# Kernel tuning notes

Hardware: AMD Instinct MI355X
Metric: run time of the kernel (lower is better)

Reference implementation:

```python
import jax, jax.numpy as jnp
import numpy as np

NEG_SLOPE = 0.2  # PyG GATConv default negative_slope


def gat_conv(x, src, dst, W, a_src, a_dst, b, N):
    """Single PyG-style GATConv (add_self_loops already applied via src/dst).
    x: [N, F_in], W: [F_in, H*C], a_src/a_dst: [H, C], b: [H*C].
    Returns [N, H*C] (concat=True)."""
    H, C = a_src.shape
    h = (x @ W).reshape(N, H, C)                      # [N,H,C]
    alpha_src = jnp.sum(h * a_src[None], axis=-1)      # [N,H]
    alpha_dst = jnp.sum(h * a_dst[None], axis=-1)      # [N,H]
    e = jax.nn.leaky_relu(alpha_src[src] + alpha_dst[dst], NEG_SLOPE)  # [E,H]
    # numerically stable segment softmax over incoming edges of each dst node
    m = jax.ops.segment_max(e, dst, num_segments=N)    # [N,H]
    m = jnp.where(jnp.isfinite(m), m, 0.0)
    ex = jnp.exp(e - m[dst])                           # [E,H]
    den = jax.ops.segment_sum(ex, dst, num_segments=N) # [N,H]
    alpha = ex / (den[dst] + 1e-16)                    # [E,H]
    out = jax.ops.segment_sum(h[src] * alpha[..., None], dst, num_segments=N)  # [N,H,C]
    return out.reshape(N, H * C) + b


def setup_inputs() -> dict:
    key = jax.random.key(0)
    ks = jax.random.split(key, 9)
    B, N, E = 2, 50000, 800000
    d_model, n_hidden, en_dim, H = 128, 128, 64, 1
    fea_mats = jax.random.normal(ks[0], (B, N, d_model), dtype=jnp.float32)
    edge_index = jax.random.randint(ks[1], (B, 2, E), 0, N, dtype=jnp.int32)
    s1 = 1.0 / np.sqrt(d_model)
    s2 = 1.0 / np.sqrt(n_hidden)
    return {
        "fea_mats": fea_mats,
        "edge_index": edge_index,
        "W1": jax.random.normal(ks[2], (d_model, H * n_hidden), dtype=jnp.float32) * s1,
        "att_src1": jax.random.normal(ks[3], (H, n_hidden), dtype=jnp.float32) * s2,
        "att_dst1": jax.random.normal(ks[4], (H, n_hidden), dtype=jnp.float32) * s2,
        "b1": jnp.zeros((H * n_hidden,), dtype=jnp.float32),
        "W2": jax.random.normal(ks[5], (H * n_hidden, H * en_dim), dtype=jnp.float32) * s2,
        "att_src2": jax.random.normal(ks[6], (H, en_dim), dtype=jnp.float32) / np.sqrt(en_dim),
        "att_dst2": jax.random.normal(ks[7], (H, en_dim), dtype=jnp.float32) / np.sqrt(en_dim),
        "b2": jnp.zeros((H * en_dim,), dtype=jnp.float32),
    }


def reference(fea_mats, edge_index, W1, att_src1, att_dst1, b1, W2, att_src2, att_dst2, b2):
    B, N, _ = fea_mats.shape
    loops = jnp.arange(N, dtype=edge_index.dtype)

    def per_graph(x, ei):
        # PyG GATConv adds self-loops by default
        src = jnp.concatenate([ei[0], loops])
        dst = jnp.concatenate([ei[1], loops])
        h = gat_conv(x, src, dst, W1, att_src1, att_dst1, b1, N)
        h = jax.nn.relu(h)
        h = gat_conv(h, src, dst, W2, att_src2, att_dst2, b2, N)
        return h  # [N, en_dim]

    return jax.vmap(per_graph)(fea_mats, edge_index)  # [B, N, en_dim]
```

## Files before the change

kernel.cpp:

```cpp
#include <hip/hip_runtime.h>

#define NEG_SLOPE 0.2f
static constexpr int BLK = 256;
static constexpr int EPB = 4096;
static constexpr int CAP = 6144;

typedef short bf16x8 __attribute__((ext_vector_type(8)));
typedef float f32x4  __attribute__((ext_vector_type(4)));
typedef unsigned short u16x8 __attribute__((ext_vector_type(8)));
typedef unsigned short u16x4 __attribute__((ext_vector_type(4)));

static inline int cdiv(long a, long b){ return (int)((a + b - 1) / b); }

__device__ __forceinline__ unsigned short f2bf(float f){
    unsigned u = __float_as_uint(f);
    u += 0x7fff + ((u >> 16) & 1);
    return (unsigned short)(u >> 16);
}
__device__ __forceinline__ float bf2f(unsigned short h){
    return __uint_as_float(((unsigned)h) << 16);
}
__device__ __forceinline__ float lrelu(float v){
    return v > 0.f ? v : NEG_SLOPE * v;
}

struct GP {
    const int* src; const int* dst; const float* X;
    int* gcnt; int* gbase; int* ebuf; int* rowptr; int* csrsrc;
    unsigned short* h1b; float* agg1; unsigned short* h2b;
    float *as1, *ad1, *as2, *ad2; float* outp;
};

template<int CO, int CT, bool RELU_IN, bool BF16OUT>
__device__ __forceinline__ void gemm_dev(
    int bid, const float* __restrict__ X,
    const unsigned short* __restrict__ Wt_hi, const unsigned short* __restrict__ Wt_lo,
    const float* __restrict__ avs, const float* __restrict__ avd,
    void* __restrict__ Hout, float* __restrict__ as_out, float* __restrict__ ad_out,
    int N, unsigned short* smem)
{
    constexpr int CHUNKS = CO / (CT * 16);
    constexpr int HWB = CT * 4096;
    int ch, rtb;
    if (CHUNKS == 1){ ch = 0; rtb = bid; } else { ch = bid & 1; rtb = bid >> 1; }
    int c0 = ch * (CT * 16);

    {
        const char* srch = (const char*)(Wt_hi + (size_t)c0 * 128);
        const char* srcl = (const char*)(Wt_lo + (size_t)c0 * 128);
        #pragma unroll
        for (int it = 0; it < CT * 2; ++it){
            int o = (it * 256 + (int)threadIdx.x) * 16;
            const char* sp = (o < HWB) ? (srch + o) : (srcl + (o - HWB));
            u16x8 v = *(const u16x8*)sp;
            int so = o ^ (((o >> 8) & 7) << 4);
            *(u16x8*)((char*)smem + so) = v;
        }
    }
    __syncthreads();

    int wave = threadIdx.x >> 6;
    int lane = threadIdx.x & 63;
    int rt = rtb * 4 + wave;
    if (rt >= (N >> 4)) return;
    int r0 = rt << 4;
    int rl = lane & 15, g = lane >> 4;
    const float* xrow = X + (long)(r0 + rl) * 128 + g * 8;

    f32x4 acc[CT];
    #pragma unroll
    for (int t = 0; t < CT; t++) acc[t] = (f32x4)(0.f);

    int sw = (rl & 7) << 4;
    #pragma unroll
    for (int ks = 0; ks < 4; ks++){
        float4 xa = *(const float4*)(xrow + ks * 32);
        float4 xb = *(const float4*)(xrow + ks * 32 + 4);
        float xv[8] = {xa.x, xa.y, xa.z, xa.w, xb.x, xb.y, xb.z, xb.w};
        bf16x8 xbf;
        #pragma unroll
        for (int j = 0; j < 8; j++){
            float x = xv[j];
            if (RELU_IN) x = fmaxf(x, 0.f);
            xbf[j] = (short)f2bf(x);
        }
        int rbase = rl * 256 + ks * 64 + g * 16;
        #pragma unroll
        for (int t = 0; t < CT; t++){
            bf16x8 wh = *(const bf16x8*)((char*)smem + ((t * 4096 + rbase) ^ sw));
            bf16x8 wl = *(const bf16x8*)((char*)smem + ((HWB + t * 4096 + rbase) ^ sw));
            acc[t] = __builtin_amdgcn_mfma_f32_16x16x32_bf16(wh, xbf, acc[t], 0, 0, 0);
            acc[t] = __builtin_amdgcn_mfma_f32_16x16x32_bf16(wl, xbf, acc[t], 0, 0, 0);
        }
    }

    float ps = 0.f, pd = 0.f;
    #pragma unroll
    for (int t = 0; t < CT; t++){
        int c = c0 + t * 16 + 4 * g;
        float4 vs4 = *(const float4*)(avs + c);
        float4 vd4 = *(const float4*)(avd + c);
        ps += acc[t][0]*vs4.x + acc[t][1]*vs4.y + acc[t][2]*vs4.z + acc[t][3]*vs4.w;
        pd += acc[t][0]*vd4.x + acc[t][1]*vd4.y + acc[t][2]*vd4.z + acc[t][3]*vd4.w;
        long base = (long)(r0 + rl) * CO + c;
        if (BF16OUT){
            u16x4 pk;
            #pragma unroll
            for (int r = 0; r < 4; r++) pk[r] = f2bf(acc[t][r]);
            *(u16x4*)((unsigned short*)Hout + base) = pk;
        } else {
            float4 pv;
            pv.x = acc[t][0]; pv.y = acc[t][1]; pv.z = acc[t][2]; pv.w = acc[t][3];
            *(float4*)((float*)Hout + base) = pv;
        }
    }
    ps += __shfl_xor(ps, 16, 64); ps += __shfl_xor(ps, 32, 64);
    pd += __shfl_xor(pd, 16, 64); pd += __shfl_xor(pd, 32, 64);
    if (g == 0){
        unsafeAtomicAdd(as_out + r0 + rl, ps);
        unsafeAtomicAdd(ad_out + r0 + rl, pd);
    }
}

__device__ __forceinline__ void bucket_dev(
    int bid, const GP* __restrict__ g, int E, int Etot, int nbk, unsigned short* smem)
{
    int* spk   = (int*)smem;
    int* shist = spk + 4096;
    int* sbase = shist + 256;
    int tid = (int)threadIdx.x;
    for (int i = tid; i < nbk; i += 256) shist[i] = 0;
    __syncthreads();
    int e0 = bid * EPB;
    #pragma unroll
    for (int i = 0; i < EPB / 256; i++){
        int idx = i * 256 + tid; int e = e0 + idx;
        unsigned p = 0xFFFFFFFFu;
        if (e < Etot){
            int s, d;
            if (e < E){ s = g->src[e]; d = g->dst[e]; } else { s = e - E; d = s; }
            p = ((unsigned)s << 16) | (unsigned)d;
            atomicAdd(&shist[d >> 8], 1);
        }
        spk[idx] = (int)p;
    }
    __syncthreads();
    for (int i = tid; i < nbk; i += 256){
        sbase[i] = atomicAdd(&g->gcnt[i], shist[i]);
        shist[i] = 0;
    }
    __syncthreads();
    #pragma unroll
    for (int i = 0; i < EPB / 256; i++){
        int idx = i * 256 + tid;
        unsigned p = (unsigned)spk[idx];
        if (p != 0xFFFFFFFFu){
            int d = (int)(p & 0xFFFFu); int b = d >> 8;
            int r = sbase[b] + atomicAdd(&shist[b], 1);
            if (r < CAP) g->ebuf[(size_t)b * CAP + r] = (int)p;
        }
    }
}

__device__ __forceinline__ void fine_dev(int k, const GP* __restrict__ g, int N, int Etot)
{
    __shared__ int pk2[CAP];
    __shared__ int fs[256];
    __shared__ int fill[256];
    __shared__ int fh[256];
    int tid = (int)threadIdx.x;
    int cnt = min(g->gcnt[k], CAP);
    int bb  = g->gbase[k];
    for (int i = tid; i < cnt; i += 256) pk2[i] = g->ebuf[(size_t)k * CAP + i];
    fh[tid] = 0; fill[tid] = 0;
    __syncthreads();
    for (int i = tid; i < cnt; i += 256) atomicAdd(&fh[pk2[i] & 255], 1);
    __syncthreads();
    int v = fh[tid];
    fs[tid] = v;
    __syncthreads();
    #pragma unroll
    for (int off = 1; off < 256; off <<= 1){
        int t = (tid >= off) ? fs[tid - off] : 0;
        __syncthreads();
        fs[tid] += t;
        __syncthreads();
    }
    int excl = fs[tid] - v;
    __syncthreads();
    fs[tid] = excl;
    __syncthreads();
    int node = k * 256 + tid;
    if (node < N) g->rowptr[node] = bb + excl;
    if (k == 0 && tid == 0) g->rowptr[N] = Etot;
    for (int i = tid; i < cnt; i += 256){
        unsigned p = (unsigned)pk2[i];
        int f = (int)(p & 255u);
        int r = atomicAdd(&fill[f], 1);
        g->csrsrc[bb + fs[f] + r] = (int)(p >> 16);
    }
}

template<int CO>
__device__ __forceinline__ void agg_dev(
    int bid, const int* __restrict__ rowptr, const int* __restrict__ csr_src,
    const float* __restrict__ as, const float* __restrict__ ad,
    const unsigned short* __restrict__ hb, const float* __restrict__ bias,
    float* __restrict__ out, int N)
{
    constexpr int GRP = (CO == 128) ? 16 : 8;
    constexpr int ELEMS = 8;
    constexpr int NPB = 256 / GRP;
    using uvec = u16x8;
    int tid = (int)threadIdx.x;
    int grp = tid / GRP;
    int ql  = tid % GRP;
    int node = bid * NPB + grp;
    if (node >= N) return;
    int start = rowptr[node];
    int deg   = rowptr[node + 1] - start;
    float adv = ad[node];

    int sv[4]; float ev[4];
    #pragma unroll
    for (int q = 0; q < 4; q++){
        int idx = q * GRP + ql;
        sv[q] = 0; ev[q] = -1e30f;
        if (idx < deg){ sv[q] = csr_src[start + idx]; ev[q] = lrelu(as[sv[q]] + adv); }
    }
    float m = fmaxf(fmaxf(ev[0], ev[1]), fmaxf(ev[2], ev[3]));
    if (deg > 4 * GRP){
        for (int j = 4 * GRP + ql; j < deg; j += GRP)
            m = fmaxf(m, lrelu(as[csr_src[start + j]] + adv));
    }
    #pragma unroll
    for (int off = GRP >> 1; off; off >>= 1) m = fmaxf(m, __shfl_xor(m, off, GRP));

    float xq[4]; float sum = 0.f;
    #pragma unroll
    for (int q = 0; q < 4; q++){
        xq[q] = (q * GRP + ql < deg) ? __expf(ev[q] - m) : 0.f;
        sum += xq[q];
    }
    if (deg > 4 * GRP){
        for (int j = 4 * GRP + ql; j < deg; j += GRP)
            sum += __expf(lrelu(as[csr_src[start + j]] + adv) - m);
    }
    #pragma unroll
    for (int off = GRP >> 1; off; off >>= 1) sum += __shfl_xor(sum, off, GRP);
    float inv = 1.f / (sum + 1e-16f);
    float av[4];
    #pragma unroll
    for (int q = 0; q < 4; q++) av[q] = xq[q] * inv;

    float acc[ELEMS];
    #pragma unroll
    for (int i = 0; i < ELEMS; i++) acc[i] = 0.f;

    #pragma unroll
    for (int q = 0; q < 4; q++){
        int rem = deg - q * GRP;
        if (rem <= 0) break;
        int lim = rem < GRP ? rem : GRP;
        float aq = av[q]; int sq = sv[q];
        int t = 0;
        for (; t + 7 < lim; t += 8){
            int   s0 = __shfl(sq, t+0, GRP), s1 = __shfl(sq, t+1, GRP);
            int   s2 = __shfl(sq, t+2, GRP), s3 = __shfl(sq, t+3, GRP);
            int   s4 = __shfl(sq, t+4, GRP), s5 = __shfl(sq, t+5, GRP);
            int   s6 = __shfl(sq, t+6, GRP), s7 = __shfl(sq, t+7, GRP);
            float a0 = __shfl(aq, t+0, GRP), a1 = __shfl(aq, t+1, GRP);
            float a2 = __shfl(aq, t+2, GRP), a3 = __shfl(aq, t+3, GRP);
            float a4 = __shfl(aq, t+4, GRP), a5 = __shfl(aq, t+5, GRP);
            float a6 = __shfl(aq, t+6, GRP), a7 = __shfl(aq, t+7, GRP);
            uvec r0 = *(const uvec*)(hb + (long)s0 * CO + ql * ELEMS);
            uvec r1 = *(const uvec*)(hb + (long)s1 * CO + ql * ELEMS);
            uvec r2 = *(const uvec*)(hb + (long)s2 * CO + ql * ELEMS);
            uvec r3 = *(const uvec*)(hb + (long)s3 * CO + ql * ELEMS);
            uvec r4 = *(const uvec*)(hb + (long)s4 * CO + ql * ELEMS);
            uvec r5 = *(const uvec*)(hb + (long)s5 * CO + ql * ELEMS);
            uvec r6 = *(const uvec*)(hb + (long)s6 * CO + ql * ELEMS);
            uvec r7 = *(const uvec*)(hb + (long)s7 * CO + ql * ELEMS);
            #pragma unroll
            for (int i = 0; i < ELEMS; i++)
                acc[i] += a0 * bf2f(r0[i]) + a1 * bf2f(r1[i])
                        + a2 * bf2f(r2[i]) + a3 * bf2f(r3[i])
                        + a4 * bf2f(r4[i]) + a5 * bf2f(r5[i])
                        + a6 * bf2f(r6[i]) + a7 * bf2f(r7[i]);
        }
        for (; t + 3 < lim; t += 4){
            int   s0 = __shfl(sq, t+0, GRP), s1 = __shfl(sq, t+1, GRP);
            int   s2 = __shfl(sq, t+2, GRP), s3 = __shfl(sq, t+3, GRP);
            float a0 = __shfl(aq, t+0, GRP), a1 = __shfl(aq, t+1, GRP);
            float a2 = __shfl(aq, t+2, GRP), a3 = __shfl(aq, t+3, GRP);
            uvec r0 = *(const uvec*)(hb + (long)s0 * CO + ql * ELEMS);
            uvec r1 = *(const uvec*)(hb + (long)s1 * CO + ql * ELEMS);
            uvec r2 = *(const uvec*)(hb + (long)s2 * CO + ql * ELEMS);
            uvec r3 = *(const uvec*)(hb + (long)s3 * CO + ql * ELEMS);
            #pragma unroll
            for (int i = 0; i < ELEMS; i++)
                acc[i] += a0 * bf2f(r0[i]) + a1 * bf2f(r1[i])
                        + a2 * bf2f(r2[i]) + a3 * bf2f(r3[i]);
        }
        for (; t < lim; t++){
            int   s0 = __shfl(sq, t, GRP);
            float a0 = __shfl(aq, t, GRP);
            uvec r0 = *(const uvec*)(hb + (long)s0 * CO + ql * ELEMS);
            #pragma unroll
            for (int i = 0; i < ELEMS; i++) acc[i] += a0 * bf2f(r0[i]);
        }
        if (lim < GRP) break;
    }
    if (deg > 4 * GRP){
        for (int j = 4 * GRP; j < deg; j++){
            int sj = csr_src[start + j];
            float aj = __expf(lrelu(as[sj] + adv) - m) * inv;
            uvec r0 = *(const uvec*)(hb + (long)sj * CO + ql * ELEMS);
            #pragma unroll
            for (int i = 0; i < ELEMS; i++) acc[i] += aj * bf2f(r0[i]);
        }
    }

    float* o = out + (long)node * CO + ql * ELEMS;
    #pragma unroll
    for (int i = 0; i < ELEMS; i += 4){
        float4 ov;
        ov.x = acc[i+0] + bias[ql * ELEMS + i + 0];
        ov.y = acc[i+1] + bias[ql * ELEMS + i + 1];
        ov.z = acc[i+2] + bias[ql * ELEMS + i + 2];
        ov.w = acc[i+3] + bias[ql * ELEMS + i + 3];
        *(float4*)(o + i) = ov;
    }
}

__global__ __launch_bounds__(BLK) void prep_k(
    const float* __restrict__ W1, const float* __restrict__ W2,
    unsigned short* __restrict__ w1h, unsigned short* __restrict__ w1l,
    unsigned short* __restrict__ w2h, unsigned short* __restrict__ w2l)
{
    int i = blockIdx.x * BLK + threadIdx.x;
    if (i < 128 * 128){
        int c = i >> 7, k = i & 127;
        float w = W1[k * 128 + c];
        unsigned short hi = f2bf(w);
        w1h[i] = hi; w1l[i] = f2bf(w - bf2f(hi));
        if (i < 64 * 128){
            float w2 = W2[k * 64 + c];
            unsigned short hi2 = f2bf(w2);
            w2h[i] = hi2; w2l[i] = f2bf(w2 - bf2f(hi2));
        }
    }
}

__global__ __launch_bounds__(256, 4) void kA(
    GP a, GP b, const unsigned short* __restrict__ w1h, const unsigned short* __restrict__ w1l,
    const float* __restrict__ avs1, const float* __restrict__ avd1,
    int EB_a, int EB_b, int GB_a, int GB_b, int E, int Etot, int N, int nbk)
{
    __shared__ unsigned short smem[16384];
    int bid = blockIdx.x;
    if (bid < EB_a){ bucket_dev(bid, &a, E, Etot, nbk, smem); return; }
    bid -= EB_a;
    if (bid < EB_b){ bucket_dev(bid, &b, E, Etot, nbk, smem); return; }
    bid -= EB_b;
    if (bid < GB_a){ gemm_dev<128,4,false,true>(bid, a.X, w1h, w1l, avs1, avd1, a.h1b, a.as1, a.ad1, N, smem); return; }
    bid -= GB_a;
    if (bid < GB_b) gemm_dev<128,4,false,true>(bid, b.X, w1h, w1l, avs1, avd1, b.h1b, b.as1, b.ad1, N, smem);
}

__global__ __launch_bounds__(256) void kscan(GP a, GP b, int nbk){
    const GP* g = (blockIdx.x == 0) ? &a : &b;
    __shared__ int sh[256];
    int tid = (int)threadIdx.x;
    int v = (tid < nbk) ? g->gcnt[tid] : 0;
    sh[tid] = v;
    __syncthreads();
    #pragma unroll
    for (int off = 1; off < 256; off <<= 1){
        int t = (tid >= off) ? sh[tid - off] : 0;
        __syncthreads();
        sh[tid] += t;
        __syncthreads();
    }
    if (tid < nbk) g->gbase[tid] = sh[tid] - v;
}

__global__ __launch_bounds__(256) void kB(GP a, GP b, int nb_a, int nb_b, int N, int Etot){
    int bid = blockIdx.x; const GP* g; int k;
    if (bid < nb_a){ g = &a; k = bid; }
    else { k = bid - nb_a; if (k >= nb_b) return; g = &b; }
    fine_dev(k, g, N, Etot);
}

__global__ __launch_bounds__(256, 4) void gemm2_k(
    GP a, GP b, const unsigned short* __restrict__ w2h, const unsigned short* __restrict__ w2l,
    const float* __restrict__ avs2, const float* __restrict__ avd2, int GB_a, int GB_b, int N)
{
    __shared__ unsigned short smem[8192];
    int bid = blockIdx.x;
    if (bid < GB_a) gemm_dev<64,2,true,true>(bid, a.agg1, w2h, w2l, avs2, avd2, a.h2b, a.as2, a.ad2, N, smem);
    else { bid -= GB_a; if (bid < GB_b) gemm_dev<64,2,true,true>(bid, b.agg1, w2h, w2l, avs2, avd2, b.h2b, b.as2, b.ad2, N, smem); }
}

template<int CO>
__global__ __launch_bounds__(BLK) void agg2_k(GP a, GP b, const float* bias, int AB_a, int AB_b, int N){
    int bid = blockIdx.x; const GP* g; int lb;
    if (bid < AB_a){ g = &a; lb = bid; }
    else { lb = bid - AB_a; if (lb >= AB_b) return; g = &b; }
    const float* as; const float* ad; const unsigned short* h; float* outp;
    if constexpr (CO == 128){ as = g->as1; ad = g->ad1; h = g->h1b; outp = g->agg1; }
    else                    { as = g->as2; ad = g->ad2; h = g->h2b; outp = g->outp; }
    agg_dev<CO>(lb, g->rowptr, g->csrsrc, as, ad, h, bias, outp, N);
}

extern "C" void kernel_launch(void* const* d_in, const int* in_sizes, int n_in,
                              void* d_out, int out_size, void* d_ws, size_t ws_size,
                              hipStream_t stream)
{
    const float* fea  = (const float*)d_in[0];
    const int*   ei   = (const int*)  d_in[1];
    const float* W1   = (const float*)d_in[2];
    const float* av_s1= (const float*)d_in[3];
    const float* av_d1= (const float*)d_in[4];
    const float* b1   = (const float*)d_in[5];
    const float* W2   = (const float*)d_in[6];
    const float* av_s2= (const float*)d_in[7];
    const float* av_d2= (const float*)d_in[8];
    const float* b2   = (const float*)d_in[9];
    float* out = (float*)d_out;

    const int B = 2;
    const int N = out_size / (B * 64);
    const int E = in_sizes[1] / (2 * B);
    const int Etot = E + N;
    const int nbk = (N + 255) >> 8;

    size_t pg = 256 + (size_t)nbk * CAP + (size_t)(N + 2) + (size_t)Etot
              + (size_t)N * (64 + 128 + 32);
    size_t wtf = 8192 + 8192 + 4096 + 4096;
    auto total_f = [&](int ng){ return wtf + (size_t)ng * (4 * (size_t)N + 256) + (size_t)ng * pg + 64; };
    bool fused = (ws_size >= total_f(2) * sizeof(float));
    int NG = fused ? 2 : 1;

    float* ws = (float*)d_ws;
    size_t off = 0;
    unsigned short* w1h = (unsigned short*)(ws + off); off += 8192;
    unsigned short* w1l = (unsigned short*)(ws + off); off += 8192;
    unsigned short* w2h = (unsigned short*)(ws + off); off += 4096;
    unsigned short* w2l = (unsigned short*)(ws + off); off += 4096;

    float* zbase = ws + off;
    size_t znum = (size_t)NG * (4 * (size_t)N + 256);
    off += znum;

    GP g[2];
    for (int gi = 0; gi < NG; gi++){
        GP p;
        p.as1  = zbase + (size_t)gi * (4 * (size_t)N + 256);
        p.ad1  = p.as1 + N;
        p.as2  = p.ad1 + N;
        p.ad2  = p.as2 + N;
        p.gcnt = (int*)(p.ad2 + N);
        p.gbase  = (int*)(ws + off); off += 256;
        p.ebuf   = (int*)(ws + off); off += (size_t)nbk * CAP;
        p.rowptr = (int*)(ws + off); off += (size_t)(N + 2);
        p.csrsrc = (int*)(ws + off); off += Etot;
        p.h1b  = (unsigned short*)(ws + off); off += (size_t)N * 64;
        p.agg1 = ws + off; off += (size_t)N * 128;
        p.h2b  = (unsigned short*)(ws + off); off += (size_t)N * 32;
        g[gi] = p;
    }

    const int RT  = N >> 4;
    const int GB1 = cdiv(RT, 4) * 2;
    const int GB2 = cdiv(RT, 4) * 2;
    const int EBk = cdiv(Etot, EPB);
    const int AB1 = cdiv(N, 16);
    const int AB2 = cdiv(N, 32);

    if (fused){
        for (int bi = 0; bi < 2; bi++){
            g[bi].src = ei + (size_t)bi * 2 * E;
            g[bi].dst = g[bi].src + E;
            g[bi].X   = fea + (size_t)bi * N * 128;
            g[bi].outp= out + (size_t)bi * N * 64;
        }
        hipMemsetAsync(zbase, 0, znum * sizeof(float), stream);
        prep_k<<<cdiv(128*128, BLK), BLK, 0, stream>>>(W1, W2, w1h, w1l, w2h, w2l);
        kA<<<2*EBk + 2*GB1, 256, 0, stream>>>(g[0], g[1], w1h, w1l, av_s1, av_d1,
                                              EBk, EBk, GB1, GB1, E, Etot, N, nbk);
        kscan<<<2, 256, 0, stream>>>(g[0], g[1], nbk);
        kB<<<2*nbk, 256, 0, stream>>>(g[0], g[1], nbk, nbk, N, Etot);
        agg2_k<128><<<2*AB1, BLK, 0, stream>>>(g[0], g[1], b1, AB1, AB1, N);
        gemm2_k <<<2*GB2, 256, 0, stream>>>(g[0], g[1], w2h, w2l, av_s2, av_d2, GB2, GB2, N);
        agg2_k<64> <<<2*AB2, BLK, 0, stream>>>(g[0], g[1], b2, AB2, AB2, N);
    } else {
        prep_k<<<cdiv(128*128, BLK), BLK, 0, stream>>>(W1, W2, w1h, w1l, w2h, w2l);
        for (int bi = 0; bi < B; bi++){
            GP p = g[0];
            p.src = ei + (size_t)bi * 2 * E;
            p.dst = p.src + E;
            p.X   = fea + (size_t)bi * N * 128;
            p.outp= out + (size_t)bi * N * 64;
            hipMemsetAsync(zbase, 0, znum * sizeof(float), stream);
            kA<<<EBk + GB1, 256, 0, stream>>>(p, p, w1h, w1l, av_s1, av_d1,
                                              EBk, 0, GB1, 0, E, Etot, N, nbk);
            kscan<<<1, 256, 0, stream>>>(p, p, nbk);
            kB<<<nbk, 256, 0, stream>>>(p, p, nbk, 0, N, Etot);
            agg2_k<128><<<AB1, BLK, 0, stream>>>(p, p, b1, AB1, 0, N);
            gemm2_k <<<GB2, 256, 0, stream>>>(p, p, w2h, w2l, av_s2, av_d2, GB2, 0, N);
            agg2_k<64> <<<AB2, BLK, 0, stream>>>(p, p, b2, AB2, 0, N);
        }
    }
}
```

Measured before the change: 223.6 us.

## Fuse layer-1 aggregation with layer-2 GEMM via LDS MFMA tile

The layer-1 aggregation kernel now applies bias and ReLU, stores the 16-node result tile in LDS as bf16, and multiplies it directly by W2 using MFMA. It writes h2 in bf16 and accumulates the layer-2 attention logits with atomics. This removes the fp32 agg1 intermediate buffer, its global write and read, and one kernel launch. The 8-wide unrolled gather loop is also dropped in favour of the 4-wide path. The trade-offs are extra MFMA work and W2 loads in every aggregation block, atomic contention on as2/ad2, and possibly less memory-level parallelism in the gather.

After: 204.2 us. 8.7% less time.

```diff
diff --git a/kernel.cpp b/kernel.cpp
--- a/kernel.cpp
+++ b/kernel.cpp
@@ -27,7 +27,7 @@
 struct GP {
     const int* src; const int* dst; const float* X;
     int* gcnt; int* gbase; int* ebuf; int* rowptr; int* csrsrc;
-    unsigned short* h1b; float* agg1; unsigned short* h2b;
+    unsigned short* h1b; unsigned short* h2b;
     float *as1, *ad1, *as2, *ad2; float* outp;
 };
 
@@ -201,22 +201,12 @@
     }
 }
 
-template<int CO>
-__device__ __forceinline__ void agg_dev(
-    int bid, const int* __restrict__ rowptr, const int* __restrict__ csr_src,
+template<int CO, int GRP>
+__device__ __forceinline__ void agg_core(
+    const int* __restrict__ rowptr, const int* __restrict__ csr_src,
     const float* __restrict__ as, const float* __restrict__ ad,
-    const unsigned short* __restrict__ hb, const float* __restrict__ bias,
-    float* __restrict__ out, int N)
-{
-    constexpr int GRP = (CO == 128) ? 16 : 8;
-    constexpr int ELEMS = 8;
-    constexpr int NPB = 256 / GRP;
-    using uvec = u16x8;
-    int tid = (int)threadIdx.x;
-    int grp = tid / GRP;
-    int ql  = tid % GRP;
-    int node = bid * NPB + grp;
-    if (node >= N) return;
+    const unsigned short* __restrict__ hb, int node, int ql, float* acc)
+{
     int start = rowptr[node];
     int deg   = rowptr[node + 1] - start;
     float adv = ad[node];
@@ -249,65 +239,37 @@
     #pragma unroll
     for (int off = GRP >> 1; off; off >>= 1) sum += __shfl_xor(sum, off, GRP);
     float inv = 1.f / (sum + 1e-16f);
-    float av[4];
-    #pragma unroll
-    for (int q = 0; q < 4; q++) av[q] = xq[q] * inv;
-
-    float acc[ELEMS];
-    #pragma unroll
-    for (int i = 0; i < ELEMS; i++) acc[i] = 0.f;
+
+    #pragma unroll
+    for (int i = 0; i < 8; i++) acc[i] = 0.f;
 
     #pragma unroll
     for (int q = 0; q < 4; q++){
         int rem = deg - q * GRP;
         if (rem <= 0) break;
         int lim = rem < GRP ? rem : GRP;
-        float aq = av[q]; int sq = sv[q];
+        float aq = xq[q] * inv; int sq = sv[q];
         int t = 0;
-        for (; t + 7 < lim; t += 8){
-            int   s0 = __shfl(sq, t+0, GRP), s1 = __shfl(sq, t+1, GRP);
-            int   s2 = __shfl(sq, t+2, GRP), s3 = __shfl(sq, t+3, GRP);
-            int   s4 = __shfl(sq, t+4, GRP), s5 = __shfl(sq, t+5, GRP);
-            int   s6 = __shfl(sq, t+6, GRP), s7 = __shfl(sq, t+7, GRP);
-            float a0 = __shfl(aq, t+0, GRP), a1 = __shfl(aq, t+1, GRP);
-            float a2 = __shfl(aq, t+2, GRP), a3 = __shfl(aq, t+3, GRP);
-            float a4 = __shfl(aq, t+4, GRP), a5 = __shfl(aq, t+5, GRP);
-            float a6 = __shfl(aq, t+6, GRP), a7 = __shfl(aq, t+7, GRP);
-            uvec r0 = *(const uvec*)(hb + (long)s0 * CO + ql * ELEMS);
-            uvec r1 = *(const uvec*)(hb + (long)s1 * CO + ql * ELEMS);
-            uvec r2 = *(const uvec*)(hb + (long)s2 * CO + ql * ELEMS);
-            uvec r3 = *(const uvec*)(hb + (long)s3 * CO + ql * ELEMS);
-            uvec r4 = *(const uvec*)(hb + (long)s4 * CO + ql * ELEMS);
-            uvec r5 = *(const uvec*)(hb + (long)s5 * CO + ql * ELEMS);
-            uvec r6 = *(const uvec*)(hb + (long)s6 * CO + ql * ELEMS);
-            uvec r7 = *(const uvec*)(hb + (long)s7 * CO + ql * ELEMS);
-            #pragma unroll
-            for (int i = 0; i < ELEMS; i++)
-                acc[i] += a0 * bf2f(r0[i]) + a1 * bf2f(r1[i])
-                        + a2 * bf2f(r2[i]) + a3 * bf2f(r3[i])
-                        + a4 * bf2f(r4[i]) + a5 * bf2f(r5[i])
-                        + a6 * bf2f(r6[i]) + a7 * bf2f(r7[i]);
-        }
         for (; t + 3 < lim; t += 4){
             int   s0 = __shfl(sq, t+0, GRP), s1 = __shfl(sq, t+1, GRP);
             int   s2 = __shfl(sq, t+2, GRP), s3 = __shfl(sq, t+3, GRP);
             float a0 = __shfl(aq, t+0, GRP), a1 = __shfl(aq, t+1, GRP);
             float a2 = __shfl(aq, t+2, GRP), a3 = __shfl(aq, t+3, GRP);
-            uvec r0 = *(const uvec*)(hb + (long)s0 * CO + ql * ELEMS);
-            uvec r1 = *(const uvec*)(hb + (long)s1 * CO + ql * ELEMS);
-            uvec r2 = *(const uvec*)(hb + (long)s2 * CO + ql * ELEMS);
-            uvec r3 = *(const uvec*)(hb + (long)s3 * CO + ql * ELEMS);
+            u16x8 r0 = *(const u16x8*)(hb + (long)s0 * CO + ql * 8);
+            u16x8 r1 = *(const u16x8*)(hb + (long)s1 * CO + ql * 8);
+            u16x8 r2 = *(const u16x8*)(hb + (long)s2 * CO + ql * 8);
+            u16x8 r3 = *(const u16x8*)(hb + (long)s3 * CO + ql * 8);
             #pragma unroll
-            for (int i = 0; i < ELEMS; i++)
+            for (int i = 0; i < 8; i++)
                 acc[i] += a0 * bf2f(r0[i]) + a1 * bf2f(r1[i])
                         + a2 * bf2f(r2[i]) + a3 * bf2f(r3[i]);
         }
         for (; t < lim; t++){
             int   s0 = __shfl(sq, t, GRP);
             float a0 = __shfl(aq, t, GRP);
-            uvec r0 = *(const uvec*)(hb + (long)s0 * CO + ql * ELEMS);
+            u16x8 r0 = *(const u16x8*)(hb + (long)s0 * CO + ql * 8);
             #pragma unroll
-            for (int i = 0; i < ELEMS; i++) acc[i] += a0 * bf2f(r0[i]);
+            for (int i = 0; i < 8; i++) acc[i] += a0 * bf2f(r0[i]);
         }
         if (lim < GRP) break;
     }
@@ -315,21 +277,10 @@
         for (int j = 4 * GRP; j < deg; j++){
             int sj = csr_src[start + j];
             float aj = __expf(lrelu(as[sj] + adv) - m) * inv;
-            uvec r0 = *(const uvec*)(hb + (long)sj * CO + ql * ELEMS);
+            u16x8 r0 = *(const u16x8*)(hb + (long)sj * CO + ql * 8);
             #pragma unroll
-            for (int i = 0; i < ELEMS; i++) acc[i] += aj * bf2f(r0[i]);
-        }
-    }
-
-    float* o = out + (long)node * CO + ql * ELEMS;
-    #pragma unroll
-    for (int i = 0; i < ELEMS; i += 4){
-        float4 ov;
-        ov.x = acc[i+0] + bias[ql * ELEMS + i + 0];
-        ov.y = acc[i+1] + bias[ql * ELEMS + i + 1];
-        ov.z = acc[i+2] + bias[ql * ELEMS + i + 2];
-        ov.w = acc[i+3] + bias[ql * ELEMS + i + 3];
-        *(float4*)(o + i) = ov;
+            for (int i = 0; i < 8; i++) acc[i] += aj * bf2f(r0[i]);
+        }
     }
 }
 
@@ -392,25 +343,90 @@
     fine_dev(k, g, N, Etot);
 }
 
-__global__ __launch_bounds__(256, 4) void gemm2_k(
-    GP a, GP b, const unsigned short* __restrict__ w2h, const unsigned short* __restrict__ w2l,
-    const float* __restrict__ avs2, const float* __restrict__ avd2, int GB_a, int GB_b, int N)
-{
-    __shared__ unsigned short smem[8192];
-    int bid = blockIdx.x;
-    if (bid < GB_a) gemm_dev<64,2,true,true>(bid, a.agg1, w2h, w2l, avs2, avd2, a.h2b, a.as2, a.ad2, N, smem);
-    else { bid -= GB_a; if (bid < GB_b) gemm_dev<64,2,true,true>(bid, b.agg1, w2h, w2l, avs2, avd2, b.h2b, b.as2, b.ad2, N, smem); }
-}
-
-template<int CO>
-__global__ __launch_bounds__(BLK) void agg2_k(GP a, GP b, const float* bias, int AB_a, int AB_b, int N){
-    int bid = blockIdx.x; const GP* g; int lb;
-    if (bid < AB_a){ g = &a; lb = bid; }
-    else { lb = bid - AB_a; if (lb >= AB_b) return; g = &b; }
-    const float* as; const float* ad; const unsigned short* h; float* outp;
-    if constexpr (CO == 128){ as = g->as1; ad = g->ad1; h = g->h1b; outp = g->agg1; }
-    else                    { as = g->as2; ad = g->ad2; h = g->h2b; outp = g->outp; }
-    agg_dev<CO>(lb, g->rowptr, g->csrsrc, as, ad, h, bias, outp, N);
+__global__ __launch_bounds__(BLK) void agg1f_k(
+    GP a, GP b, const float* __restrict__ b1,
+    const unsigned short* __restrict__ w2h, const unsigned short* __restrict__ w2l,
+    const float* __restrict__ avs2, const float* __restrict__ avd2,
+    int AB_a, int AB_b, int N)
+{
+    __shared__ unsigned short xlds[16 * 128];
+    int bid = blockIdx.x; const GP* g;
+    if (bid < AB_a){ g = &a; }
+    else { bid -= AB_a; if (bid >= AB_b) return; g = &b; }
+    int tid = (int)threadIdx.x;
+    int grp = tid >> 4, ql = tid & 15;
+    int node = bid * 16 + grp;
+
+    {
+        u16x8 xv;
+        if (node < N){
+            float acc[8];
+            agg_core<128,16>(g->rowptr, g->csrsrc, g->as1, g->ad1, g->h1b, node, ql, acc);
+            #pragma unroll
+            for (int i = 0; i < 8; i++)
+                xv[i] = f2bf(fmaxf(acc[i] + b1[ql * 8 + i], 0.f));
+        } else {
+            #pragma unroll
+            for (int i = 0; i < 8; i++) xv[i] = 0;
+        }
+        int bo = (grp * 256 + ql * 16) ^ ((grp & 7) << 4);
+        *(u16x8*)((char*)xlds + bo) = xv;
+    }
+    __syncthreads();
+
+    int lane = tid & 63, wv = tid >> 6;
+    int rl = lane & 15, kg = lane >> 4;
+    f32x4 d = (f32x4)(0.f);
+    #pragma unroll
+    for (int kb = 0; kb < 4; kb++){
+        bf16x8 af = *(const bf16x8*)((char*)xlds + ((rl * 256 + kb * 64 + kg * 16) ^ ((rl & 7) << 4)));
+        long wo = (long)(wv * 16 + rl) * 128 + kb * 32 + kg * 8;
+        bf16x8 bh = *(const bf16x8*)(w2h + wo);
+        bf16x8 bl = *(const bf16x8*)(w2l + wo);
+        d = __builtin_amdgcn_mfma_f32_16x16x32_bf16(af, bh, d, 0, 0, 0);
+        d = __builtin_amdgcn_mfma_f32_16x16x32_bf16(af, bl, d, 0, 0, 0);
+    }
+    float pvs = avs2[wv * 16 + rl], pvd = avd2[wv * 16 + rl];
+    #pragma unroll
+    for (int reg = 0; reg < 4; reg++){
+        int nd = bid * 16 + 4 * kg + reg;
+        float hv = d[reg];
+        if (nd < N) g->h2b[(long)nd * 64 + wv * 16 + rl] = f2bf(hv);
+        float s_ = hv * pvs, d_ = hv * pvd;
+        #pragma unroll
+        for (int off = 1; off < 16; off <<= 1){
+            s_ += __shfl_xor(s_, off, 16);
+            d_ += __shfl_xor(d_, off, 16);
+        }
+        if (rl == 0 && nd < N){
+            unsafeAtomicAdd(g->as2 + nd, s_);
+            unsafeAtomicAdd(g->ad2 + nd, d_);
+        }
+    }
+}
+
+__global__ __launch_bounds__(BLK) void agg2f_k(
+    GP a, GP b, const float* __restrict__ bias, int AB_a, int AB_b, int N)
+{
+    int bid = blockIdx.x; const GP* g;
+    if (bid < AB_a){ g = &a; }
+    else { bid -= AB_a; if (bid >= AB_b) return; g = &b; }
+    int tid = (int)threadIdx.x;
+    int grp = tid >> 3, ql = tid & 7;
+    int node = bid * 32 + grp;
+    if (node >= N) return;
+    float acc[8];
+    agg_core<64,8>(g->rowptr, g->csrsrc, g->as2, g->ad2, g->h2b, node, ql, acc);
+    float* o = g->outp + (long)node * 64 + ql * 8;
+    #pragma unroll
+    for (int i = 0; i < 8; i += 4){
+        float4 ov;
+        ov.x = acc[i+0] + bias[ql * 8 + i + 0];
+        ov.y = acc[i+1] + bias[ql * 8 + i + 1];
+        ov.z = acc[i+2] + bias[ql * 8 + i + 2];
+        ov.w = acc[i+3] + bias[ql * 8 + i + 3];
+        *(float4*)(o + i) = ov;
+    }
 }
 
 extern "C" void kernel_launch(void* const* d_in, const int* in_sizes, int n_in,
@@ -436,7 +452,7 @@
     const int nbk = (N + 255) >> 8;
 
     size_t pg = 256 + (size_t)nbk * CAP + (size_t)(N + 2) + (size_t)Etot
-              + (size_t)N * (64 + 128 + 32);
+              + (size_t)N * (64 + 32);
     size_t wtf = 8192 + 8192 + 4096 + 4096;
     auto total_f = [&](int ng){ return wtf + (size_t)ng * (4 * (size_t)N + 256) + (size_t)ng * pg + 64; };
     bool fused = (ws_size >= total_f(2) * sizeof(float));
@@ -466,14 +482,12 @@
         p.rowptr = (int*)(ws + off); off += (size_t)(N + 2);
         p.csrsrc = (int*)(ws + off); off += Etot;
         p.h1b  = (unsigned short*)(ws + off); off += (size_t)N * 64;
-        p.agg1 = ws + off; off += (size_t)N * 128;
         p.h2b  = (unsigned short*)(ws + off); off += (size_t)N * 32;
         g[gi] = p;
     }
 
     const int RT  = N >> 4;
     const int GB1 = cdiv(RT, 4) * 2;
-    const int GB2 = cdiv(RT, 4) * 2;
     const int EBk = cdiv(Etot, EPB);
     const int AB1 = cdiv(N, 16);
     const int AB2 = cdiv(N, 32);
@@ -491,9 +505,8 @@
                                               EBk, EBk, GB1, GB1, E, Etot, N, nbk);
         kscan<<<2, 256, 0, stream>>>(g[0], g[1], nbk);
         kB<<<2*nbk, 256, 0, stream>>>(g[0], g[1], nbk, nbk, N, Etot);
-        agg2_k<128><<<2*AB1, BLK, 0, stream>>>(g[0], g[1], b1, AB1, AB1, N);
-        gemm2_k <<<2*GB2, 256, 0, stream>>>(g[0], g[1], w2h, w2l, av_s2, av_d2, GB2, GB2, N);
-        agg2_k<64> <<<2*AB2, BLK, 0, stream>>>(g[0], g[1], b2, AB2, AB2, N);
+        agg1f_k<<<2*AB1, BLK, 0, stream>>>(g[0], g[1], b1, w2h, w2l, av_s2, av_d2, AB1, AB1, N);
+        agg2f_k<<<2*AB2, BLK, 0, stream>>>(g[0], g[1], b2, AB2, AB2, N);
     } else {
         prep_k<<<cdiv(128*128, BLK), BLK, 0, stream>>>(W1, W2, w1h, w1l, w2h, w2l);
         for (int bi = 0; bi < B; bi++){
@@ -507,9 +520,8 @@
                                               EBk, 0, GB1, 0, E, Etot, N, nbk);
             kscan<<<1, 256, 0, stream>>>(p, p, nbk);
             kB<<<nbk, 256, 0, stream>>>(p, p, nbk, 0, N, Etot);
-            agg2_k<128><<<AB1, BLK, 0, stream>>>(p, p, b1, AB1, 0, N);
-            gemm2_k <<<GB2, 256, 0, stream>>>(p, p, w2h, w2l, av_s2, av_d2, GB2, 0, N);
-            agg2_k<64> <<<AB2, BLK, 0, stream>>>(p, p, b2, AB2, 0, N);
-        }
-    }
-}
+            agg1f_k<<<AB1, BLK, 0, stream>>>(p, p, b1, w2h, w2l, av_s2, av_d2, AB1, 0, N);
+            agg2f_k<<<AB2, BLK, 0, stream>>>(p, p, b2, AB2, 0, N);
+        }
+    }
+}
```
